# Kernel optimization log

Hardware: AMD Instinct MI355X
Metric: run time of the kernel (lower is better)

Reference implementation:

```python
import jax, jax.numpy as jnp
import numpy as np

DIM = 512
GROUPS = 8

def setup_inputs() -> dict:
    key = jax.random.key(0)
    k1, k2, k3, k4, k5 = jax.random.split(key, 5)
    B, L, C = 8, 4096, DIM
    s = 1.0 / np.sqrt(C)
    x = jax.random.normal(k1, (B, L, C), dtype=jnp.float32)
    W_qkv = jax.random.normal(k2, (C, 3 * C), dtype=jnp.float32) * s
    b_qkv = jax.random.normal(k3, (3 * C,), dtype=jnp.float32) * 0.01
    W_proj = jax.random.normal(k4, (C, C), dtype=jnp.float32) * s
    b_proj = jax.random.normal(k5, (C,), dtype=jnp.float32) * 0.01
    return {"x": x, "W_qkv": W_qkv, "b_qkv": b_qkv,
            "W_proj": W_proj, "b_proj": b_proj, "size": 64}

def reference(x, W_qkv, b_qkv, W_proj, b_proj, size):
    B, L, C = x.shape
    g = GROUPS
    hd = C // g  # per-group channel dim
    qkv = x @ W_qkv + b_qkv                       # [B, L, 3C]
    qkv = qkv.reshape(B, L, 3, g, hd).transpose(2, 0, 3, 1, 4)  # [3, B, g, L, hd]
    q, k, v = qkv[0], qkv[1], qkv[2]
    q = q * (float(L) ** -0.5)
    # channel-wise (cross-covariance) attention: [B, g, hd, hd]
    attn = jnp.einsum('bgld,bgle->bgde', q, k)
    attn = jax.nn.softmax(attn, axis=-1)
    out = jnp.einsum('bgde,bgle->bgld', attn, v)  # [B, g, L, hd]
    out = out.transpose(0, 2, 1, 3).reshape(B, L, C)
    out = out @ W_proj + b_proj
    return (out, size)
```

## Files before the change

### kernel.cpp

```cpp
#include <hip/hip_runtime.h>
#include <hip/hip_bf16.h>
#include <stdint.h>

typedef __hip_bfloat16 bf16;
typedef __attribute__((ext_vector_type(8))) short s16x8;
typedef __attribute__((ext_vector_type(4))) short s16x4;
typedef __attribute__((ext_vector_type(4))) float f32x4;

__device__ __forceinline__ short f2bf_bits(float f) {
    union { bf16 b; short s; } u; u.b = __float2bfloat16(f); return u.s;
}

__device__ __forceinline__ void gload_lds16(const void* g, void* l) {
    __builtin_amdgcn_global_load_lds(
        (const __attribute__((address_space(1))) void*)(uintptr_t)g,
        (__attribute__((address_space(3))) void*)(uintptr_t)l,
        16, 0, 0);
}

__device__ __forceinline__ f32x4 mfma16(s16x8 a, s16x8 b, f32x4 c) {
    return __builtin_amdgcn_mfma_f32_16x16x32_bf16(a, b, c, 0, 0, 0);
}

__global__ __launch_bounds__(256) void cvt_bf16_kernel(const float* __restrict__ in,
                                                       bf16* __restrict__ out, int n8) {
    int i = blockIdx.x * blockDim.x + threadIdx.x;
    int stride = gridDim.x * blockDim.x;
    for (; i < n8; i += stride) {
        f32x4 a = ((const f32x4*)in)[2 * i];
        f32x4 b = ((const f32x4*)in)[2 * i + 1];
        s16x8 o;
        o[0] = f2bf_bits(a[0]); o[1] = f2bf_bits(a[1]);
        o[2] = f2bf_bits(a[2]); o[3] = f2bf_bits(a[3]);
        o[4] = f2bf_bits(b[0]); o[5] = f2bf_bits(b[1]);
        o[6] = f2bf_bits(b[2]); o[7] = f2bf_bits(b[3]);
        ((s16x8*)out)[i] = o;
    }
}

__global__ __launch_bounds__(256) void transpose_cvt_kernel(const float* __restrict__ in,
                                                            bf16* __restrict__ out,
                                                            int R, int C) {
    __shared__ float t[32][33];
    int c0 = blockIdx.x * 32, r0 = blockIdx.y * 32;
    int lx = threadIdx.x & 31, ly = threadIdx.x >> 5;
    for (int i = ly; i < 32; i += 8)
        t[i][lx] = in[(size_t)(r0 + i) * C + (c0 + lx)];
    __syncthreads();
    for (int i = ly; i < 32; i += 8)
        out[(size_t)(c0 + i) * R + (r0 + lx)] = __float2bfloat16(t[lx][i]);
}

__global__ __launch_bounds__(256, 2) void gemm_qkv_kernel(
    const bf16* __restrict__ A, const bf16* __restrict__ Bt,
    const float* __restrict__ bias,
    bf16* __restrict__ qT, bf16* __restrict__ kT, bf16* __restrict__ V) {
    __shared__ __align__(16) char smem[33280];
    bf16* As = (bf16*)smem;
    bf16* Bs = (bf16*)(smem + 16384);
    const int tid = threadIdx.x;
    const int wid = tid >> 6, lane = tid & 63;
    const int r16 = lane & 15, rg = lane >> 4;
    const int wr = wid >> 1, wc = wid & 1;
    const int flat = blockIdx.y * 12 + blockIdx.x;
    const int nb = (flat & 7) * 384 + (flat >> 3);
    const int n0 = (nb % 12) * 128;
    const int m0 = (nb / 12) * 128;

    f32x4 acc[4][4] = {};
    for (int ks = 0; ks < 8; ++ks) {
        const int k0 = ks * 64;
#pragma unroll
        for (int it = 0; it < 4; ++it) {
            int f = (it * 256 + tid) << 4;
            int row = f >> 7;
            int sc = ((f >> 4) & 7) ^ (row & 7);
            gload_lds16((const char*)(A + (size_t)(m0 + row) * 512 + k0) + (sc << 4),
                        (char*)As + ((it * 256 + (wid << 6)) << 4));
            gload_lds16((const char*)(Bt + (size_t)(n0 + row) * 512 + k0) + (sc << 4),
                        (char*)Bs + ((it * 256 + (wid << 6)) << 4));
        }
        __syncthreads();
#pragma unroll
        for (int kk = 0; kk < 2; ++kk) {
            s16x8 af[4], bfv[4];
#pragma unroll
            for (int mi = 0; mi < 4; ++mi) {
                int row = (wr << 6) + (mi << 4) + r16;
                int off = (row << 7) + ((((kk << 2) + rg) ^ (row & 7)) << 4);
                af[mi] = *(const s16x8*)((const char*)As + off);
            }
#pragma unroll
            for (int ni = 0; ni < 4; ++ni) {
                int row = (wc << 6) + (ni << 4) + r16;
                int off = (row << 7) + ((((kk << 2) + rg) ^ (row & 7)) << 4);
                bfv[ni] = *(const s16x8*)((const char*)Bs + off);
            }
#pragma unroll
            for (int mi = 0; mi < 4; ++mi)
#pragma unroll
                for (int ni = 0; ni < 4; ++ni)
                    acc[mi][ni] = mfma16(af[mi], bfv[ni], acc[mi][ni]);
        }
        __syncthreads();
    }

    const int bb = m0 >> 12;
    const int l0 = m0 & 4095;
    const float scale = (n0 < 512) ? 0.015625f : 1.0f;
    bf16* tr = (bf16*)smem;
    float bv[4];
#pragma unroll
    for (int ni = 0; ni < 4; ++ni)
        bv[ni] = bias[n0 + (wc << 6) + (ni << 4) + r16];
#pragma unroll
    for (int mi = 0; mi < 4; ++mi)
#pragma unroll
        for (int ni = 0; ni < 4; ++ni) {
            int col = (wc << 6) + (ni << 4) + r16;
#pragma unroll
            for (int r = 0; r < 4; ++r) {
                int row = (wr << 6) + (mi << 4) + (rg << 2) + r;
                tr[row * 130 + col] = __float2bfloat16((acc[mi][ni][r] + bv[ni]) * scale);
            }
        }
    __syncthreads();
    if (n0 < 1024) {
        bf16* dst; int c0;
        if (n0 < 512) { dst = qT; c0 = n0; } else { dst = kT; c0 = n0 - 512; }
#pragma unroll 4
        for (int it = 0; it < 64; ++it) {
            int flat2 = it * 256 + tid;
            int cl = flat2 >> 7, ll = flat2 & 127;
            dst[((size_t)(bb * 512 + c0 + cl) << 12) + (l0 + ll)] = tr[ll * 130 + cl];
        }
    } else {
        int c0 = n0 - 1024;
#pragma unroll 4
        for (int it = 0; it < 64; ++it) {
            int flat2 = it * 256 + tid;
            int rr = flat2 >> 7, cc = flat2 & 127;
            V[((size_t)(m0 + rr) << 9) + (c0 + cc)] = tr[rr * 130 + cc];
        }
    }
}

__global__ __launch_bounds__(256, 2) void s_partial_kernel(
    const bf16* __restrict__ qT, const bf16* __restrict__ kT,
    float* __restrict__ S_part) {
    __shared__ __align__(16) bf16 qs[64 * 64];
    __shared__ __align__(16) bf16 ks2[64 * 64];
    const int chunk = blockIdx.x, bg = blockIdx.y;
    const int tid = threadIdx.x, wid = tid >> 6, lane = tid & 63;
    const int r16 = lane & 15, rg = lane >> 4;
    const int wr = wid >> 1, wc = wid & 1;
    const size_t base = ((size_t)bg << 18) + chunk * 256;
    const bf16* qb = qT + base;
    const bf16* kb = kT + base;
    f32x4 acc[2][2] = {};
    for (int ks = 0; ks < 4; ++ks) {
#pragma unroll
        for (int it = 0; it < 2; ++it) {
            int f = (it * 256 + tid) << 4;
            int row = f >> 7;
            int sc = ((f >> 4) & 7) ^ (row & 7);
            gload_lds16((const char*)(qb + ((size_t)row << 12) + ks * 64) + (sc << 4),
                        (char*)qs + ((it * 256 + (wid << 6)) << 4));
            gload_lds16((const char*)(kb + ((size_t)row << 12) + ks * 64) + (sc << 4),
                        (char*)ks2 + ((it * 256 + (wid << 6)) << 4));
        }
        __syncthreads();
#pragma unroll
        for (int kk = 0; kk < 2; ++kk) {
            s16x8 aq[2], bk[2];
#pragma unroll
            for (int mi = 0; mi < 2; ++mi) {
                int row = (wr << 5) + (mi << 4) + r16;
                int off = (row << 7) + ((((kk << 2) + rg) ^ (row & 7)) << 4);
                aq[mi] = *(const s16x8*)((const char*)qs + off);
            }
#pragma unroll
            for (int ni = 0; ni < 2; ++ni) {
                int row = (wc << 5) + (ni << 4) + r16;
                int off = (row << 7) + ((((kk << 2) + rg) ^ (row & 7)) << 4);
                bk[ni] = *(const s16x8*)((const char*)ks2 + off);
            }
#pragma unroll
            for (int mi = 0; mi < 2; ++mi)
#pragma unroll
                for (int ni = 0; ni < 2; ++ni)
                    acc[mi][ni] = mfma16(aq[mi], bk[ni], acc[mi][ni]);
        }
        __syncthreads();
    }
    float* o = S_part + (((size_t)chunk << 6) + bg) * 4096;
#pragma unroll
    for (int mi = 0; mi < 2; ++mi)
#pragma unroll
        for (int ni = 0; ni < 2; ++ni)
#pragma unroll
            for (int r = 0; r < 4; ++r) {
                int row = (wr << 5) + (mi << 4) + (rg << 2) + r;
                int col = (wc << 5) + (ni << 4) + r16;
                o[(row << 6) + col] = acc[mi][ni][r];
            }
}

__global__ __launch_bounds__(256) void softmax_kernel(const float* __restrict__ S_part,
                                                      bf16* __restrict__ attn) {
    const int q4 = blockIdx.x, bg = blockIdx.y;
    const int tid = threadIdx.x;
    const int dl = tid >> 4, es = tid & 15;
    const int d = (q4 << 4) + dl;
    const float* base = S_part + ((size_t)bg << 12) + (d << 6) + (es << 2);
    float s[4] = {0.f, 0.f, 0.f, 0.f};
#pragma unroll
    for (int p = 0; p < 16; ++p) {
        f32x4 v4 = *(const f32x4*)(base + ((size_t)p << 18));
        s[0] += v4[0]; s[1] += v4[1]; s[2] += v4[2]; s[3] += v4[3];
    }
    float m = fmaxf(fmaxf(s[0], s[1]), fmaxf(s[2], s[3]));
    m = fmaxf(m, __shfl_xor(m, 1));
    m = fmaxf(m, __shfl_xor(m, 2));
    m = fmaxf(m, __shfl_xor(m, 4));
    m = fmaxf(m, __shfl_xor(m, 8));
    float sum = 0.f;
#pragma unroll
    for (int j = 0; j < 4; ++j) { s[j] = __expf(s[j] - m); sum += s[j]; }
    sum += __shfl_xor(sum, 1);
    sum += __shfl_xor(sum, 2);
    sum += __shfl_xor(sum, 4);
    sum += __shfl_xor(sum, 8);
    float inv = 1.0f / sum;
    s16x4 w;
#pragma unroll
    for (int j = 0; j < 4; ++j) w[j] = f2bf_bits(s[j] * inv);
    *(s16x4*)(attn + ((size_t)bg << 12) + (d << 6) + (es << 2)) = w;
}

__global__ __launch_bounds__(256, 2) void pv_kernel(const bf16* __restrict__ V,
                                                    const bf16* __restrict__ attn,
                                                    bf16* __restrict__ aout) {
    const int lc = blockIdx.x, bg = blockIdx.y;
    const int b = bg >> 3, g = bg & 7;
    const int tid = threadIdx.x, wid = tid >> 6, lane = tid & 63;
    const int r16 = lane & 15, rg = lane >> 4;
    const bf16* ab = attn + ((size_t)bg << 12);
    s16x8 bfr[4][2];
#pragma unroll
    for (int ni = 0; ni < 4; ++ni)
#pragma unroll
        for (int kk = 0; kk < 2; ++kk)
            bfr[ni][kk] = *(const s16x8*)(ab + (((ni << 4) + r16) << 6) + (kk << 5) + (rg << 3));
    const size_t mrow = (size_t)b * 4096 + lc * 256 + wid * 64;
    const bf16* vb = V + (mrow << 9) + (g << 6);
    f32x4 acc[4][4] = {};
#pragma unroll
    for (int mi = 0; mi < 4; ++mi) {
#pragma unroll
        for (int kk = 0; kk < 2; ++kk) {
            s16x8 af = *(const s16x8*)(vb + (((size_t)(mi << 4) + r16) << 9) + (kk << 5) + (rg << 3));
#pragma unroll
            for (int ni = 0; ni < 4; ++ni)
                acc[mi][ni] = mfma16(af, bfr[ni][kk], acc[mi][ni]);
        }
    }
    bf16* ob = aout + (mrow << 9) + (g << 6);
#pragma unroll
    for (int mi = 0; mi < 4; ++mi)
#pragma unroll
        for (int ni = 0; ni < 4; ++ni)
#pragma unroll
            for (int r = 0; r < 4; ++r)
                ob[((size_t)((mi << 4) + (rg << 2) + r) << 9) + (ni << 4) + r16] =
                    __float2bfloat16(acc[mi][ni][r]);
}

__global__ __launch_bounds__(256, 2) void gemm_proj_kernel(
    const bf16* __restrict__ A, const bf16* __restrict__ Bt,
    const float* __restrict__ bias, float* __restrict__ out) {
    __shared__ __align__(16) char smem[32768];
    bf16* As = (bf16*)smem;
    bf16* Bs = (bf16*)(smem + 16384);
    const int tid = threadIdx.x;
    const int wid = tid >> 6, lane = tid & 63;
    const int r16 = lane & 15, rg = lane >> 4;
    const int wr = wid >> 1, wc = wid & 1;
    const int flat = blockIdx.y * 4 + blockIdx.x;
    const int nb = (flat & 7) * 128 + (flat >> 3);
    const int n0 = (nb & 3) * 128;
    const int m0 = (nb >> 2) * 128;
    f32x4 acc[4][4] = {};
    for (int ks = 0; ks < 8; ++ks) {
        const int k0 = ks * 64;
#pragma unroll
        for (int it = 0; it < 4; ++it) {
            int f = (it * 256 + tid) << 4;
            int row = f >> 7;
            int sc = ((f >> 4) & 7) ^ (row & 7);
            gload_lds16((const char*)(A + (size_t)(m0 + row) * 512 + k0) + (sc << 4),
                        (char*)As + ((it * 256 + (wid << 6)) << 4));
            gload_lds16((const char*)(Bt + (size_t)(n0 + row) * 512 + k0) + (sc << 4),
                        (char*)Bs + ((it * 256 + (wid << 6)) << 4));
        }
        __syncthreads();
#pragma unroll
        for (int kk = 0; kk < 2; ++kk) {
            s16x8 af[4], bfv[4];
#pragma unroll
            for (int mi = 0; mi < 4; ++mi) {
                int row = (wr << 6) + (mi << 4) + r16;
                int off = (row << 7) + ((((kk << 2) + rg) ^ (row & 7)) << 4);
                af[mi] = *(const s16x8*)((const char*)As + off);
            }
#pragma unroll
            for (int ni = 0; ni < 4; ++ni) {
                int row = (wc << 6) + (ni << 4) + r16;
                int off = (row << 7) + ((((kk << 2) + rg) ^ (row & 7)) << 4);
                bfv[ni] = *(const s16x8*)((const char*)Bs + off);
            }
#pragma unroll
            for (int mi = 0; mi < 4; ++mi)
#pragma unroll
                for (int ni = 0; ni < 4; ++ni)
                    acc[mi][ni] = mfma16(af[mi], bfv[ni], acc[mi][ni]);
        }
        __syncthreads();
    }
    float bv[4];
#pragma unroll
    for (int ni = 0; ni < 4; ++ni)
        bv[ni] = bias[n0 + (wc << 6) + (ni << 4) + r16];
#pragma unroll
    for (int mi = 0; mi < 4; ++mi)
#pragma unroll
        for (int ni = 0; ni < 4; ++ni)
#pragma unroll
            for (int r = 0; r < 4; ++r)
                out[(size_t)(m0 + (wr << 6) + (mi << 4) + (rg << 2) + r) * 512 +
                    (n0 + (wc << 6) + (ni << 4) + r16)] = acc[mi][ni][r] + bv[ni];
}

__global__ void tail_kernel(const int* __restrict__ sz, float* __restrict__ out) {
    out[0] = (float)sz[0];
}

extern "C" void kernel_launch(void* const* d_in, const int* in_sizes, int n_in,
                              void* d_out, int out_size, void* d_ws, size_t ws_size,
                              hipStream_t stream) {
    const float* x      = (const float*)d_in[0];
    const float* W_qkv  = (const float*)d_in[1];
    const float* b_qkv  = (const float*)d_in[2];
    const float* W_proj = (const float*)d_in[3];
    const float* b_proj = (const float*)d_in[4];
    const int*   size_p = (const int*)d_in[5];
    float* out = (float*)d_out;

    char* ws = (char*)d_ws;
    bf16* xb      = (bf16*)ws;
    bf16* Wqkv_t  = (bf16*)(ws + 33554432);
    bf16* Wproj_t = (bf16*)(ws + 35127296);
    bf16* qT      = (bf16*)(ws + 35651584);
    bf16* kT      = (bf16*)(ws + 69206016);
    bf16* V       = (bf16*)(ws + 102760448);
    float* S_part = (float*)xb;
    bf16*  attn   = (bf16*)(ws + 16777216);
    bf16*  aout   = qT;

    cvt_bf16_kernel<<<dim3(2048), dim3(256), 0, stream>>>(x, xb, 2097152);
    transpose_cvt_kernel<<<dim3(48, 16), dim3(256), 0, stream>>>(W_qkv, Wqkv_t, 512, 1536);
    transpose_cvt_kernel<<<dim3(16, 16), dim3(256), 0, stream>>>(W_proj, Wproj_t, 512, 512);
    gemm_qkv_kernel<<<dim3(12, 256), dim3(256), 0, stream>>>(xb, Wqkv_t, b_qkv, qT, kT, V);
    s_partial_kernel<<<dim3(16, 64), dim3(256), 0, stream>>>(qT, kT, S_part);
    softmax_kernel<<<dim3(4, 64), dim3(256), 0, stream>>>(S_part, attn);
    pv_kernel<<<dim3(16, 64), dim3(256), 0, stream>>>(V, attn, aout);
    gemm_proj_kernel<<<dim3(4, 256), dim3(256), 0, stream>>>(aout, Wproj_t, b_proj, out);
    tail_kernel<<<1, 1, 0, stream>>>(size_p, out + (out_size - 1));
    (void)in_sizes; (void)n_in; (void)ws_size;
}
```

Baseline: 260.9 us.

## Fold attention into per-batch projection weights and fuse x conversion into QKV GEMM

Precomputes a per-batch effective projection weight Weff = blockdiag(attn) @ W_proj, so the PV kernel and the aout round trip disappear and the output GEMM reads V directly. The fp32-to-bf16 conversion of x moves into the QKV GEMM's A-tile load, which drops the separate conversion pass and its 32MB intermediate. The weight transposes and the tail write are merged into one prep kernel, cutting launches. In exchange the A loads now go through registers instead of direct-to-LDS, and Weff is rounded to bf16, which adds a little numerical error.

```diff
diff --git a/kernel.cpp b/kernel.cpp
--- a/kernel.cpp
+++ b/kernel.cpp
@@ -22,37 +22,29 @@
     return __builtin_amdgcn_mfma_f32_16x16x32_bf16(a, b, c, 0, 0, 0);
 }
 
-__global__ __launch_bounds__(256) void cvt_bf16_kernel(const float* __restrict__ in,
-                                                       bf16* __restrict__ out, int n8) {
-    int i = blockIdx.x * blockDim.x + threadIdx.x;
-    int stride = gridDim.x * blockDim.x;
-    for (; i < n8; i += stride) {
-        f32x4 a = ((const f32x4*)in)[2 * i];
-        f32x4 b = ((const f32x4*)in)[2 * i + 1];
-        s16x8 o;
-        o[0] = f2bf_bits(a[0]); o[1] = f2bf_bits(a[1]);
-        o[2] = f2bf_bits(a[2]); o[3] = f2bf_bits(a[3]);
-        o[4] = f2bf_bits(b[0]); o[5] = f2bf_bits(b[1]);
-        o[6] = f2bf_bits(b[2]); o[7] = f2bf_bits(b[3]);
-        ((s16x8*)out)[i] = o;
-    }
-}
-
-__global__ __launch_bounds__(256) void transpose_cvt_kernel(const float* __restrict__ in,
-                                                            bf16* __restrict__ out,
-                                                            int R, int C) {
+__global__ __launch_bounds__(256) void prep_kernel(const float* __restrict__ Wq,
+                                                   const float* __restrict__ Wp,
+                                                   bf16* __restrict__ Wqt,
+                                                   bf16* __restrict__ Wpt,
+                                                   const int* __restrict__ sz,
+                                                   float* __restrict__ tailout) {
+    if (blockIdx.x == 0 && blockIdx.y == 0 && threadIdx.x == 0)
+        tailout[0] = (float)sz[0];
     __shared__ float t[32][33];
-    int c0 = blockIdx.x * 32, r0 = blockIdx.y * 32;
+    const float* in; bf16* out; int C, c0;
+    if (blockIdx.x < 48) { in = Wq; out = Wqt; C = 1536; c0 = blockIdx.x * 32; }
+    else                 { in = Wp; out = Wpt; C = 512;  c0 = (blockIdx.x - 48) * 32; }
+    int r0 = blockIdx.y * 32;
     int lx = threadIdx.x & 31, ly = threadIdx.x >> 5;
     for (int i = ly; i < 32; i += 8)
         t[i][lx] = in[(size_t)(r0 + i) * C + (c0 + lx)];
     __syncthreads();
     for (int i = ly; i < 32; i += 8)
-        out[(size_t)(c0 + i) * R + (r0 + lx)] = __float2bfloat16(t[lx][i]);
+        out[(size_t)(c0 + i) * 512 + (r0 + lx)] = __float2bfloat16(t[lx][i]);
 }
 
 __global__ __launch_bounds__(256, 2) void gemm_qkv_kernel(
-    const bf16* __restrict__ A, const bf16* __restrict__ Bt,
+    const float* __restrict__ X, const bf16* __restrict__ Bt,
     const float* __restrict__ bias,
     bf16* __restrict__ qT, bf16* __restrict__ kT, bf16* __restrict__ V) {
     __shared__ __align__(16) char smem[33280];
@@ -75,10 +67,22 @@
             int f = (it * 256 + tid) << 4;
             int row = f >> 7;
             int sc = ((f >> 4) & 7) ^ (row & 7);
-            gload_lds16((const char*)(A + (size_t)(m0 + row) * 512 + k0) + (sc << 4),
-                        (char*)As + ((it * 256 + (wid << 6)) << 4));
             gload_lds16((const char*)(Bt + (size_t)(n0 + row) * 512 + k0) + (sc << 4),
                         (char*)Bs + ((it * 256 + (wid << 6)) << 4));
+        }
+#pragma unroll
+        for (int it = 0; it < 4; ++it) {
+            int cidx = it * 256 + tid;
+            int row = cidx >> 3, c8 = cidx & 7;
+            const float* src = X + (size_t)(m0 + row) * 512 + k0 + (c8 << 3);
+            f32x4 a = *(const f32x4*)src;
+            f32x4 b = *(const f32x4*)(src + 4);
+            s16x8 o;
+            o[0] = f2bf_bits(a[0]); o[1] = f2bf_bits(a[1]);
+            o[2] = f2bf_bits(a[2]); o[3] = f2bf_bits(a[3]);
+            o[4] = f2bf_bits(b[0]); o[5] = f2bf_bits(b[1]);
+            o[6] = f2bf_bits(b[2]); o[7] = f2bf_bits(b[3]);
+            *(s16x8*)((char*)As + (row << 7) + ((c8 ^ (row & 7)) << 4)) = o;
         }
         __syncthreads();
 #pragma unroll
@@ -207,7 +211,7 @@
 }
 
 __global__ __launch_bounds__(256) void softmax_kernel(const float* __restrict__ S_part,
-                                                      bf16* __restrict__ attn) {
+                                                      bf16* __restrict__ attnT) {
     const int q4 = blockIdx.x, bg = blockIdx.y;
     const int tid = threadIdx.x;
     const int dl = tid >> 4, es = tid & 15;
@@ -232,52 +236,78 @@
     sum += __shfl_xor(sum, 4);
     sum += __shfl_xor(sum, 8);
     float inv = 1.0f / sum;
-    s16x4 w;
-#pragma unroll
-    for (int j = 0; j < 4; ++j) w[j] = f2bf_bits(s[j] * inv);
-    *(s16x4*)(attn + ((size_t)bg << 12) + (d << 6) + (es << 2)) = w;
-}
-
-__global__ __launch_bounds__(256, 2) void pv_kernel(const bf16* __restrict__ V,
-                                                    const bf16* __restrict__ attn,
-                                                    bf16* __restrict__ aout) {
-    const int lc = blockIdx.x, bg = blockIdx.y;
-    const int b = bg >> 3, g = bg & 7;
+    bf16* ob = attnT + ((size_t)bg << 12) + d;
+#pragma unroll
+    for (int j = 0; j < 4; ++j)
+        ob[((es << 2) + j) << 6] = __float2bfloat16(s[j] * inv);
+}
+
+__global__ __launch_bounds__(256, 2) void weff_kernel(
+    const bf16* __restrict__ attnT, const bf16* __restrict__ Wpt,
+    bf16* __restrict__ WeffT) {
+    __shared__ __align__(16) bf16 As[64 * 64];
+    __shared__ __align__(16) bf16 Bs[128 * 64];
+    const int c0 = blockIdx.x * 128, b = blockIdx.y;
     const int tid = threadIdx.x, wid = tid >> 6, lane = tid & 63;
     const int r16 = lane & 15, rg = lane >> 4;
-    const bf16* ab = attn + ((size_t)bg << 12);
-    s16x8 bfr[4][2];
-#pragma unroll
-    for (int ni = 0; ni < 4; ++ni)
-#pragma unroll
-        for (int kk = 0; kk < 2; ++kk)
-            bfr[ni][kk] = *(const s16x8*)(ab + (((ni << 4) + r16) << 6) + (kk << 5) + (rg << 3));
-    const size_t mrow = (size_t)b * 4096 + lc * 256 + wid * 64;
-    const bf16* vb = V + (mrow << 9) + (g << 6);
-    f32x4 acc[4][4] = {};
-#pragma unroll
-    for (int mi = 0; mi < 4; ++mi) {
+    const int wr = wid >> 1, wc = wid & 1;
+    bf16* Wout = WeffT + ((size_t)b << 18);
+    for (int g = 0; g < 8; ++g) {
+        const bf16* at = attnT + ((size_t)(b * 8 + g) << 12);
+#pragma unroll
+        for (int it = 0; it < 2; ++it) {
+            int cidx = it * 256 + tid;
+            int row = cidx >> 3, c8 = cidx & 7;
+            gload_lds16(at + (row << 6) + ((c8 ^ (row & 7)) << 3),
+                        (char*)As + ((it * 256 + (wid << 6)) << 4));
+        }
+#pragma unroll
+        for (int it = 0; it < 4; ++it) {
+            int cidx = it * 256 + tid;
+            int row = cidx >> 3, c8 = cidx & 7;
+            gload_lds16(Wpt + (size_t)(c0 + row) * 512 + (g << 6) + ((c8 ^ (row & 7)) << 3),
+                        (char*)Bs + ((it * 256 + (wid << 6)) << 4));
+        }
+        __syncthreads();
+        f32x4 acc[2][4] = {};
 #pragma unroll
         for (int kk = 0; kk < 2; ++kk) {
-            s16x8 af = *(const s16x8*)(vb + (((size_t)(mi << 4) + r16) << 9) + (kk << 5) + (rg << 3));
-#pragma unroll
-            for (int ni = 0; ni < 4; ++ni)
-                acc[mi][ni] = mfma16(af, bfr[ni][kk], acc[mi][ni]);
-        }
-    }
-    bf16* ob = aout + (mrow << 9) + (g << 6);
-#pragma unroll
-    for (int mi = 0; mi < 4; ++mi)
-#pragma unroll
-        for (int ni = 0; ni < 4; ++ni)
-#pragma unroll
-            for (int r = 0; r < 4; ++r)
-                ob[((size_t)((mi << 4) + (rg << 2) + r) << 9) + (ni << 4) + r16] =
-                    __float2bfloat16(acc[mi][ni][r]);
-}
-
-__global__ __launch_bounds__(256, 2) void gemm_proj_kernel(
-    const bf16* __restrict__ A, const bf16* __restrict__ Bt,
+            s16x8 af[2], bfv[4];
+#pragma unroll
+            for (int mi = 0; mi < 2; ++mi) {
+                int row = (wr << 5) + (mi << 4) + r16;
+                int off = (row << 7) + ((((kk << 2) + rg) ^ (row & 7)) << 4);
+                af[mi] = *(const s16x8*)((const char*)As + off);
+            }
+#pragma unroll
+            for (int ni = 0; ni < 4; ++ni) {
+                int row = (wc << 6) + (ni << 4) + r16;
+                int off = (row << 7) + ((((kk << 2) + rg) ^ (row & 7)) << 4);
+                bfv[ni] = *(const s16x8*)((const char*)Bs + off);
+            }
+#pragma unroll
+            for (int mi = 0; mi < 2; ++mi)
+#pragma unroll
+                for (int ni = 0; ni < 4; ++ni)
+                    acc[mi][ni] = mfma16(af[mi], bfv[ni], acc[mi][ni]);
+        }
+        __syncthreads();
+#pragma unroll
+        for (int mi = 0; mi < 2; ++mi)
+#pragma unroll
+            for (int ni = 0; ni < 4; ++ni) {
+                int c = c0 + (wc << 6) + (ni << 4) + r16;
+                int e0 = (wr << 5) + (mi << 4) + (rg << 2);
+                s16x4 w;
+#pragma unroll
+                for (int r = 0; r < 4; ++r) w[r] = f2bf_bits(acc[mi][ni][r]);
+                *(s16x4*)(Wout + (size_t)c * 512 + (g << 6) + e0) = w;
+            }
+    }
+}
+
+__global__ __launch_bounds__(256, 2) void gemm_out_kernel(
+    const bf16* __restrict__ A, const bf16* __restrict__ WeffT,
     const float* __restrict__ bias, float* __restrict__ out) {
     __shared__ __align__(16) char smem[32768];
     bf16* As = (bf16*)smem;
@@ -290,6 +320,7 @@
     const int nb = (flat & 7) * 128 + (flat >> 3);
     const int n0 = (nb & 3) * 128;
     const int m0 = (nb >> 2) * 128;
+    const bf16* Bt = WeffT + ((size_t)(m0 >> 12) << 18);
     f32x4 acc[4][4] = {};
     for (int ks = 0; ks < 8; ++ks) {
         const int k0 = ks * 64;
@@ -339,10 +370,6 @@
             for (int r = 0; r < 4; ++r)
                 out[(size_t)(m0 + (wr << 6) + (mi << 4) + (rg << 2) + r) * 512 +
                     (n0 + (wc << 6) + (ni << 4) + r16)] = acc[mi][ni][r] + bv[ni];
-}
-
-__global__ void tail_kernel(const int* __restrict__ sz, float* __restrict__ out) {
-    out[0] = (float)sz[0];
 }
 
 extern "C" void kernel_launch(void* const* d_in, const int* in_sizes, int n_in,
@@ -357,24 +384,21 @@
     float* out = (float*)d_out;
 
     char* ws = (char*)d_ws;
-    bf16* xb      = (bf16*)ws;
-    bf16* Wqkv_t  = (bf16*)(ws + 33554432);
-    bf16* Wproj_t = (bf16*)(ws + 35127296);
-    bf16* qT      = (bf16*)(ws + 35651584);
-    bf16* kT      = (bf16*)(ws + 69206016);
-    bf16* V       = (bf16*)(ws + 102760448);
-    float* S_part = (float*)xb;
-    bf16*  attn   = (bf16*)(ws + 16777216);
-    bf16*  aout   = qT;
-
-    cvt_bf16_kernel<<<dim3(2048), dim3(256), 0, stream>>>(x, xb, 2097152);
-    transpose_cvt_kernel<<<dim3(48, 16), dim3(256), 0, stream>>>(W_qkv, Wqkv_t, 512, 1536);
-    transpose_cvt_kernel<<<dim3(16, 16), dim3(256), 0, stream>>>(W_proj, Wproj_t, 512, 512);
-    gemm_qkv_kernel<<<dim3(12, 256), dim3(256), 0, stream>>>(xb, Wqkv_t, b_qkv, qT, kT, V);
+    bf16*  Wqkv_t  = (bf16*)ws;
+    bf16*  Wproj_t = (bf16*)(ws + 1572864);
+    bf16*  qT      = (bf16*)(ws + 2097152);
+    bf16*  kT      = (bf16*)(ws + 35651584);
+    bf16*  V       = (bf16*)(ws + 69206016);
+    float* S_part  = (float*)(ws + 102760448);
+    bf16*  attnT   = (bf16*)(ws + 119537664);
+    bf16*  WeffT   = (bf16*)(ws + 120061952);
+
+    prep_kernel<<<dim3(64, 16), dim3(256), 0, stream>>>(W_qkv, W_proj, Wqkv_t, Wproj_t,
+                                                        size_p, out + (out_size - 1));
+    gemm_qkv_kernel<<<dim3(12, 256), dim3(256), 0, stream>>>(x, Wqkv_t, b_qkv, qT, kT, V);
     s_partial_kernel<<<dim3(16, 64), dim3(256), 0, stream>>>(qT, kT, S_part);
-    softmax_kernel<<<dim3(4, 64), dim3(256), 0, stream>>>(S_part, attn);
-    pv_kernel<<<dim3(16, 64), dim3(256), 0, stream>>>(V, attn, aout);
-    gemm_proj_kernel<<<dim3(4, 256), dim3(256), 0, stream>>>(aout, Wproj_t, b_proj, out);
-    tail_kernel<<<1, 1, 0, stream>>>(size_p, out + (out_size - 1));
+    softmax_kernel<<<dim3(4, 64), dim3(256), 0, stream>>>(S_part, attnT);
+    weff_kernel<<<dim3(4, 8), dim3(256), 0, stream>>>(attnT, Wproj_t, WeffT);
+    gemm_out_kernel<<<dim3(4, 256), dim3(256), 0, stream>>>(V, WeffT, b_proj, out);
     (void)in_sizes; (void)n_in; (void)ws_size;
 }
```

New measurement: 271.9 us. 4.2% more time.
